# Kernel tuning notes

Hardware: AMD Instinct MI355X
Metric: run time of the kernel (lower is better)

Reference implementation:

```python
import jax, jax.numpy as jnp
import numpy as np

WINDOW = 21
PATCH = 1
H_PARAM = 0.1
EPS = 1e-10


def _box_sum(x, w):
    # Sum over a w x w sliding window (VALID), per (batch, channel).
    return jax.lax.reduce_window(x, 0.0, jax.lax.add,
                                 (1, 1, w, w), (1, 1, 1, 1), 'VALID')


def setup_inputs() -> dict:
    key = jax.random.key(0)
    noisy = jax.random.uniform(key, (8, 3, 512, 512), dtype=jnp.float32)
    return {"noisy": noisy}


def reference(noisy) -> jnp.ndarray:
    # Faithful vectorization of the per-pixel loop for patch_size=1.
    # For each pixel p=(i,j):
    #   window = padded[i:i+W, j:j+W]; center = noisy[i,j]
    #   dists  = mean((window - center)^2)
    #   weights = exp(-dists / h^2)            # shape (B, C)
    #   patch  = window[0, 0] = padded[i, j]   # top-left of window (half_patch=0)
    #   out[:, c, i, j] = sum_b weights[b,c] * patch[b,c]   (sum over BATCH)
    #   wsum[:, c, i, j] = sum_b weights[b,c]
    # out = clamp(out / (wsum + 1e-10), 0, 1)
    h2 = H_PARAM * H_PARAM
    W = WINDOW
    pad = W // 2
    B, C, Hh, Ww = noisy.shape
    padded = jnp.pad(noisy, ((0, 0), (0, 0), (pad, pad), (pad, pad)), mode='reflect')

    # mean((window - center)^2) = (S2 - 2*center*S1 + W^2*center^2) / W^2
    s1 = _box_sum(padded, W)                  # (B, C, H, W)
    s2 = _box_sum(padded * padded, W)
    n_win = jnp.asarray(W * W, dtype=noisy.dtype)
    dists = (s2 - 2.0 * noisy * s1 + n_win * noisy * noisy) / n_win

    weights = jnp.exp(-dists / h2)            # (B, C, H, W)
    patch = padded[:, :, :Hh, :Ww]            # top-left pixel of each window

    num = jnp.sum(weights * patch, axis=0, keepdims=True)   # (1, C, H, W)
    den = jnp.sum(weights, axis=0, keepdims=True)
    out = num / (den + EPS)
    out = jnp.broadcast_to(out, noisy.shape)  # loop assigns same row to all b
    return jnp.clip(out, 0.0, 1.0)
```

## Files before the change

kernel.cpp:

```cpp
#include <hip/hip_runtime.h>

#define B 8
#define CCH 3
#define HH 512
#define WW 512
#define WIN 21
#define PAD 10
#define TSX 32
#define TSY 32
#define PTY 52
#define TROW 60
#define HSH 53
#define NSLOT 676

__device__ __forceinline__ void lds_barrier() {
    asm volatile("s_waitcnt lgkmcnt(0)" ::: "memory");
    __builtin_amdgcn_s_barrier();
    asm volatile("" ::: "memory");
}

__global__ __launch_bounds__(256, 3) void nlm_fused_kernel(const float* __restrict__ noisy,
                                                           float* __restrict__ out) {
    __shared__ float  tile[2][PTY][TROW];
    __shared__ float2 hs_t[2][TSX][HSH];

    const int tid = threadIdx.x;
    const int x0 = blockIdx.x * TSX;
    const int y0 = blockIdx.y * TSY;
    const int ch = blockIdx.z;

    int   rowbase[3], gxs[3];
    float* ldsp[3];
    bool  valid[3], edge[3];
    #pragma unroll
    for (int k = 0; k < 3; ++k) {
        int s = tid + 256 * k;
        valid[k] = (s < NSLOT);
        int ss = valid[k] ? s : 0;
        int r  = ss / 13;
        int c4 = ss - r * 13;
        int gy = y0 + r - PAD;
        gy = (gy < 0) ? -gy : ((gy >= HH) ? (2 * (HH - 1) - gy) : gy);
        int gx = x0 + (c4 << 2) - PAD;
        rowbase[k] = gy * WW;
        gxs[k]     = gx;
        edge[k]    = (gx < 0) || (gx > WW - 4);
        ldsp[k]    = &tile[0][r][c4 << 2];
    }

    const float* src0 = noisy + (size_t)ch * (HH * WW);
    float4 pre[3];
    #pragma unroll
    for (int k = 0; k < 3; ++k) {
        if (valid[k]) {
            if (!edge[k]) {
                pre[k] = *(const float4*)(src0 + rowbase[k] + gxs[k]);
            } else {
                float tmp[4];
                #pragma unroll
                for (int t = 0; t < 4; ++t) {
                    int gx = gxs[k] + t;
                    gx = (gx < 0) ? -gx : ((gx >= WW) ? (2 * (WW - 1) - gx) : gx);
                    tmp[t] = src0[rowbase[k] + gx];
                }
                pre[k] = make_float4(tmp[0], tmp[1], tmp[2], tmp[3]);
            }
        }
    }

    float num[4] = {0.f, 0.f, 0.f, 0.f};
    float den[4] = {0.f, 0.f, 0.f, 0.f};

    const int tx  = tid & 31;
    const int ty0 = (tid >> 5) << 2;
    const float kE = (-100.0f / 441.0f) * 1.44269504088896f;

    int par = 0;
    for (int b = 0; b < B; ++b) {
        #pragma unroll
        for (int k = 0; k < 3; ++k)
            if (valid[k]) *(float4*)(ldsp[k] + par * (PTY * TROW)) = pre[k];
        lds_barrier();

        if (b < B - 1) {
            const float* srcn = noisy + (size_t)((b + 1) * CCH + ch) * (HH * WW);
            #pragma unroll
            for (int k = 0; k < 3; ++k) {
                if (valid[k]) {
                    if (!edge[k]) {
                        pre[k] = *(const float4*)(srcn + rowbase[k] + gxs[k]);
                    } else {
                        float tmp[4];
                        #pragma unroll
                        for (int t = 0; t < 4; ++t) {
                            int gx = gxs[k] + t;
                            gx = (gx < 0) ? -gx : ((gx >= WW) ? (2 * (WW - 1) - gx) : gx);
                            tmp[t] = srcn[rowbase[k] + gx];
                        }
                        pre[k] = make_float4(tmp[0], tmp[1], tmp[2], tmp[3]);
                    }
                }
            }
        }

        if (tid < PTY * 4) {
            int r   = tid >> 2;
            int cx0 = (tid & 3) << 3;
            float v[28];
            #pragma unroll
            for (int q = 0; q < 7; ++q)
                *(float4*)&v[q * 4] = *(const float4*)&tile[par][r][cx0 + (q << 2)];
            float s1 = 0.f, s2 = 0.f;
            #pragma unroll
            for (int k = 0; k <= 20; ++k) { s1 += v[k]; s2 = fmaf(v[k], v[k], s2); }
            hs_t[par][cx0][r] = make_float2(s1, s2);
            #pragma unroll
            for (int j = 1; j < 8; ++j) {
                float vo = v[j - 1], vn = v[j + 20];
                s1 += vn - vo;
                s2 += vn * vn - vo * vo;
                hs_t[par][cx0 + j][r] = make_float2(s1, s2);
            }
        }
        lds_barrier();

        float2 h0 = hs_t[par][tx][ty0];
        float2 h1 = hs_t[par][tx][ty0 + 1];
        float2 h2 = hs_t[par][tx][ty0 + 2];
        float vs1 = h0.x + h1.x + h2.x;
        float vs2 = h0.y + h1.y + h2.y;
        #pragma unroll
        for (int k = 3; k <= 20; ++k) {
            float2 h = hs_t[par][tx][ty0 + k];
            vs1 += h.x;
            vs2 += h.y;
        }
        {
            float a = tile[par][ty0 + PAD][tx + PAD];
            float p = tile[par][ty0][tx];
            float dd = fmaf(a, fmaf(441.f, a, -2.f * vs1), vs2);
            float w = exp2f(dd * kE);
            num[0] += w * p; den[0] += w;
        }
        #pragma unroll
        for (int i = 1; i < 4; ++i) {
            float2 hn = hs_t[par][tx][ty0 + 20 + i];
            float2 ho = (i == 1) ? h0 : ((i == 2) ? h1 : h2);
            vs1 += hn.x - ho.x;
            vs2 += hn.y - ho.y;
            float a = tile[par][ty0 + i + PAD][tx + PAD];
            float p = tile[par][ty0 + i][tx];
            float dd = fmaf(a, fmaf(441.f, a, -2.f * vs1), vs2);
            float w = exp2f(dd * kE);
            num[i] += w * p; den[i] += w;
        }
        par ^= 1;
    }

    #pragma unroll
    for (int i = 0; i < 4; ++i) {
        int y = y0 + ty0 + i;
        int x = x0 + tx;
        float v = num[i] / (den[i] + 1e-10f);
        v = v < 0.f ? 0.f : (v > 1.f ? 1.f : v);
        #pragma unroll
        for (int b = 0; b < B; ++b)
            out[((size_t)(b * CCH + ch) * HH + y) * WW + x] = v;
    }
}

extern "C" void kernel_launch(void* const* d_in, const int* in_sizes, int n_in,
                              void* d_out, int out_size, void* d_ws, size_t ws_size,
                              hipStream_t stream) {
    const float* noisy = (const float*)d_in[0];
    float* out = (float*)d_out;
    dim3 grid(WW / TSX, HH / TSY, CCH);
    nlm_fused_kernel<<<grid, dim3(256), 0, stream>>>(noisy, out);
}
```

Baseline: 89.09 us.

## Process two batch planes per iteration with double prefetch and split horizontal work

```diff
diff --git a/kernel.cpp b/kernel.cpp
--- a/kernel.cpp
+++ b/kernel.cpp
@@ -4,6 +4,7 @@
 #define CCH 3
 #define HH 512
 #define WW 512
+#define HW (HH * WW)
 #define WIN 21
 #define PAD 10
 #define TSX 32
@@ -12,6 +13,7 @@
 #define TROW 60
 #define HSH 53
 #define NSLOT 676
+#define HTASK (PTY * 4)
 
 __device__ __forceinline__ void lds_barrier() {
     asm volatile("s_waitcnt lgkmcnt(0)" ::: "memory");
@@ -30,7 +32,7 @@
     const int ch = blockIdx.z;
 
     int   rowbase[3], gxs[3];
-    float* ldsp[3];
+    int   ldso[3];
     bool  valid[3], edge[3];
     #pragma unroll
     for (int k = 0; k < 3; ++k) {
@@ -45,25 +47,28 @@
         rowbase[k] = gy * WW;
         gxs[k]     = gx;
         edge[k]    = (gx < 0) || (gx > WW - 4);
-        ldsp[k]    = &tile[0][r][c4 << 2];
-    }
-
-    const float* src0 = noisy + (size_t)ch * (HH * WW);
-    float4 pre[3];
+        ldso[k]    = r * TROW + (c4 << 2);
+    }
+
+    float4 pre[2][3];
     #pragma unroll
-    for (int k = 0; k < 3; ++k) {
-        if (valid[k]) {
-            if (!edge[k]) {
-                pre[k] = *(const float4*)(src0 + rowbase[k] + gxs[k]);
-            } else {
-                float tmp[4];
-                #pragma unroll
-                for (int t = 0; t < 4; ++t) {
-                    int gx = gxs[k] + t;
-                    gx = (gx < 0) ? -gx : ((gx >= WW) ? (2 * (WW - 1) - gx) : gx);
-                    tmp[t] = src0[rowbase[k] + gx];
+    for (int u = 0; u < 2; ++u) {
+        const float* src = noisy + (size_t)(u * CCH + ch) * HW;
+        #pragma unroll
+        for (int k = 0; k < 3; ++k) {
+            if (valid[k]) {
+                if (!edge[k]) {
+                    pre[u][k] = *(const float4*)(src + rowbase[k] + gxs[k]);
+                } else {
+                    float tmp[4];
+                    #pragma unroll
+                    for (int t = 0; t < 4; ++t) {
+                        int gx = gxs[k] + t;
+                        gx = (gx < 0) ? -gx : ((gx >= WW) ? (2 * (WW - 1) - gx) : gx);
+                        tmp[t] = src[rowbase[k] + gx];
+                    }
+                    pre[u][k] = make_float4(tmp[0], tmp[1], tmp[2], tmp[3]);
                 }
-                pre[k] = make_float4(tmp[0], tmp[1], tmp[2], tmp[3]);
             }
         }
     }
@@ -75,86 +80,106 @@
     const int ty0 = (tid >> 5) << 2;
     const float kE = (-100.0f / 441.0f) * 1.44269504088896f;
 
-    int par = 0;
-    for (int b = 0; b < B; ++b) {
-        #pragma unroll
-        for (int k = 0; k < 3; ++k)
-            if (valid[k]) *(float4*)(ldsp[k] + par * (PTY * TROW)) = pre[k];
+    for (int pb = 0; pb < B; pb += 2) {
         lds_barrier();
-
-        if (b < B - 1) {
-            const float* srcn = noisy + (size_t)((b + 1) * CCH + ch) * (HH * WW);
-            #pragma unroll
-            for (int k = 0; k < 3; ++k) {
-                if (valid[k]) {
-                    if (!edge[k]) {
-                        pre[k] = *(const float4*)(srcn + rowbase[k] + gxs[k]);
-                    } else {
-                        float tmp[4];
-                        #pragma unroll
-                        for (int t = 0; t < 4; ++t) {
-                            int gx = gxs[k] + t;
-                            gx = (gx < 0) ? -gx : ((gx >= WW) ? (2 * (WW - 1) - gx) : gx);
-                            tmp[t] = srcn[rowbase[k] + gx];
+        #pragma unroll
+        for (int u = 0; u < 2; ++u)
+            #pragma unroll
+            for (int k = 0; k < 3; ++k)
+                if (valid[k]) *(float4*)(&tile[u][0][0] + ldso[k]) = pre[u][k];
+        lds_barrier();
+
+        if (pb < B - 2) {
+            #pragma unroll
+            for (int u = 0; u < 2; ++u) {
+                const float* srcn = noisy + (size_t)((pb + 2 + u) * CCH + ch) * HW;
+                #pragma unroll
+                for (int k = 0; k < 3; ++k) {
+                    if (valid[k]) {
+                        if (!edge[k]) {
+                            pre[u][k] = *(const float4*)(srcn + rowbase[k] + gxs[k]);
+                        } else {
+                            float tmp[4];
+                            #pragma unroll
+                            for (int t = 0; t < 4; ++t) {
+                                int gx = gxs[k] + t;
+                                gx = (gx < 0) ? -gx : ((gx >= WW) ? (2 * (WW - 1) - gx) : gx);
+                                tmp[t] = srcn[rowbase[k] + gx];
+                            }
+                            pre[u][k] = make_float4(tmp[0], tmp[1], tmp[2], tmp[3]);
                         }
-                        pre[k] = make_float4(tmp[0], tmp[1], tmp[2], tmp[3]);
                     }
                 }
             }
         }
 
-        if (tid < PTY * 4) {
-            int r   = tid >> 2;
-            int cx0 = (tid & 3) << 3;
+        auto hwork = [&](int u, int t) {
+            int r   = t >> 2;
+            int cx0 = (t & 3) << 3;
             float v[28];
             #pragma unroll
             for (int q = 0; q < 7; ++q)
-                *(float4*)&v[q * 4] = *(const float4*)&tile[par][r][cx0 + (q << 2)];
+                *(float4*)&v[q * 4] = *(const float4*)&tile[u][r][cx0 + (q << 2)];
             float s1 = 0.f, s2 = 0.f;
             #pragma unroll
             for (int k = 0; k <= 20; ++k) { s1 += v[k]; s2 = fmaf(v[k], v[k], s2); }
-            hs_t[par][cx0][r] = make_float2(s1, s2);
+            hs_t[u][cx0][r] = make_float2(s1, s2);
             #pragma unroll
             for (int j = 1; j < 8; ++j) {
                 float vo = v[j - 1], vn = v[j + 20];
                 s1 += vn - vo;
                 s2 += vn * vn - vo * vo;
-                hs_t[par][cx0 + j][r] = make_float2(s1, s2);
+                hs_t[u][cx0 + j][r] = make_float2(s1, s2);
             }
-        }
+        };
+        if (tid < HTASK) hwork(0, tid);
+        if (tid >= 48)   hwork(1, tid - 48);
         lds_barrier();
 
-        float2 h0 = hs_t[par][tx][ty0];
-        float2 h1 = hs_t[par][tx][ty0 + 1];
-        float2 h2 = hs_t[par][tx][ty0 + 2];
-        float vs1 = h0.x + h1.x + h2.x;
-        float vs2 = h0.y + h1.y + h2.y;
+        const float2* colA = &hs_t[0][tx][0];
+        const float2* colB = &hs_t[1][tx][0];
+        float2 hA0 = colA[ty0], hA1 = colA[ty0 + 1], hA2 = colA[ty0 + 2];
+        float2 hB0 = colB[ty0], hB1 = colB[ty0 + 1], hB2 = colB[ty0 + 2];
+        float vs1A = hA0.x + hA1.x + hA2.x, vs2A = hA0.y + hA1.y + hA2.y;
+        float vs1B = hB0.x + hB1.x + hB2.x, vs2B = hB0.y + hB1.y + hB2.y;
         #pragma unroll
         for (int k = 3; k <= 20; ++k) {
-            float2 h = hs_t[par][tx][ty0 + k];
-            vs1 += h.x;
-            vs2 += h.y;
+            float2 hA = colA[ty0 + k];
+            float2 hB = colB[ty0 + k];
+            vs1A += hA.x; vs2A += hA.y;
+            vs1B += hB.x; vs2B += hB.y;
         }
         {
-            float a = tile[par][ty0 + PAD][tx + PAD];
-            float p = tile[par][ty0][tx];
-            float dd = fmaf(a, fmaf(441.f, a, -2.f * vs1), vs2);
-            float w = exp2f(dd * kE);
-            num[0] += w * p; den[0] += w;
+            float aA = tile[0][ty0 + PAD][tx + PAD];
+            float pA = tile[0][ty0][tx];
+            float aB = tile[1][ty0 + PAD][tx + PAD];
+            float pB = tile[1][ty0][tx];
+            float ddA = fmaf(aA, fmaf(441.f, aA, -2.f * vs1A), vs2A);
+            float ddB = fmaf(aB, fmaf(441.f, aB, -2.f * vs1B), vs2B);
+            float wA = exp2f(ddA * kE);
+            float wB = exp2f(ddB * kE);
+            num[0] += wA * pA; den[0] += wA;
+            num[0] += wB * pB; den[0] += wB;
         }
         #pragma unroll
         for (int i = 1; i < 4; ++i) {
-            float2 hn = hs_t[par][tx][ty0 + 20 + i];
-            float2 ho = (i == 1) ? h0 : ((i == 2) ? h1 : h2);
-            vs1 += hn.x - ho.x;
-            vs2 += hn.y - ho.y;
-            float a = tile[par][ty0 + i + PAD][tx + PAD];
-            float p = tile[par][ty0 + i][tx];
-            float dd = fmaf(a, fmaf(441.f, a, -2.f * vs1), vs2);
-            float w = exp2f(dd * kE);
-            num[i] += w * p; den[i] += w;
-        }
-        par ^= 1;
+            float2 hnA = colA[ty0 + 20 + i];
+            float2 hnB = colB[ty0 + 20 + i];
+            float2 hoA = (i == 1) ? hA0 : ((i == 2) ? hA1 : hA2);
+            float2 hoB = (i == 1) ? hB0 : ((i == 2) ? hB1 : hB2);
+            vs1A += hnA.x - hoA.x; vs2A += hnA.y - hoA.y;
+            vs1B += hnB.x - hoB.x; vs2B += hnB.y - hoB.y;
+            float aA = tile[0][ty0 + i + PAD][tx + PAD];
+            float pA = tile[0][ty0 + i][tx];
+            float aB = tile[1][ty0 + i + PAD][tx + PAD];
+            float pB = tile[1][ty0 + i][tx];
+            float ddA = fmaf(aA, fmaf(441.f, aA, -2.f * vs1A), vs2A);
+            float ddB = fmaf(aB, fmaf(441.f, aB, -2.f * vs1B), vs2B);
+            float wA = exp2f(ddA * kE);
+            float wB = exp2f(ddB * kE);
+            num[i] += wA * pA; den[i] += wA;
+            num[i] += wB * pB; den[i] += wB;
+        }
     }
 
     #pragma unroll
@@ -164,8 +189,8 @@
         float v = num[i] / (den[i] + 1e-10f);
         v = v < 0.f ? 0.f : (v > 1.f ? 1.f : v);
         #pragma unroll
-        for (int b = 0; b < B; ++b)
-            out[((size_t)(b * CCH + ch) * HH + y) * WW + x] = v;
+        for (int bb = 0; bb < B; ++bb)
+            out[((size_t)(bb * CCH + ch) * HH + y) * WW + x] = v;
     }
 }
 
```

After: 94.29 us. 1.06x slower.
